# Performance work log

Hardware: AMD Instinct MI355X
Metric: run time of the kernel (lower is better)

## Reference

```python
import jax, jax.numpy as jnp
import numpy as np

N = 50000      # nodes
E = 600000     # edges
D = 128        # embedding_dim
H = 256        # GENConv MLP hidden = 2*D (expansion=2, num_layers=2)
L = 2          # n_layers
EPS_MSG = 1e-7
EPS_NORM = 1e-5


def setup_inputs() -> dict:
    key = jax.random.key(0)
    ks = jax.random.split(key, 16)
    s = 0.05
    inp = {}
    inp["x"] = jax.random.normal(ks[0], (N, 1), jnp.float32)
    inp["edge_index"] = jax.random.randint(ks[1], (2, E), 0, N)
    inp["edge_attr"] = jax.random.normal(ks[2], (E, 1), jnp.float32)
    # encoders
    inp["Wn"] = jax.random.normal(ks[3], (1, D), jnp.float32) * s
    inp["bn_b"] = jnp.zeros((D,), jnp.float32)
    inp["We"] = jax.random.normal(ks[4], (1, D), jnp.float32) * s
    inp["be"] = jnp.zeros((D,), jnp.float32)
    # per-layer BatchNorm affine
    inp["bn_gamma"] = jnp.ones((L, D), jnp.float32)
    inp["bn_beta"] = jnp.zeros((L, D), jnp.float32)
    # per-layer GENConv params: learnable temperature t, MLP [D->H->D] with LayerNorm
    inp["t"] = jnp.ones((L,), jnp.float32)
    inp["W1"] = jax.random.normal(ks[5], (L, D, H), jnp.float32) * s
    inp["b1"] = jnp.zeros((L, H), jnp.float32)
    inp["ln_g"] = jnp.ones((L, H), jnp.float32)
    inp["ln_b"] = jnp.zeros((L, H), jnp.float32)
    inp["W2"] = jax.random.normal(ks[6], (L, H, D), jnp.float32) * s
    inp["b2"] = jnp.zeros((L, D), jnp.float32)
    return inp


def _segment_softmax(logits, seg, num):
    # per-channel softmax over edges grouped by destination node
    m = jax.ops.segment_max(logits, seg, num_segments=num)
    m = jnp.where(jnp.isfinite(m), m, 0.0)  # empty segments
    ex = jnp.exp(logits - m[seg])
    den = jax.ops.segment_sum(ex, seg, num_segments=num)
    return ex / (den[seg] + 1e-16)


def reference(x, edge_index, edge_attr, Wn, bn_b, We, be,
              bn_gamma, bn_beta, t, W1, b1, ln_g, ln_b, W2, b2):
    src, dst = edge_index[0], edge_index[1]
    h = x @ Wn + bn_b                 # [N, D] node encoder
    e = edge_attr @ We + be           # [E, D] edge encoder
    for l in range(L):
        # DeepGCNLayer 'res+': h_in -> BN -> ReLU -> conv -> + h_in
        mu = h.mean(axis=0)
        var = h.var(axis=0)
        hn = (h - mu) / jnp.sqrt(var + EPS_NORM) * bn_gamma[l] + bn_beta[l]
        hn = jax.nn.relu(hn)
        # GENConv: msg = relu(x_j + e) + eps; softmax-aggr with temperature t
        msg = jax.nn.relu(hn[src] + e) + EPS_MSG          # [E, D]
        alpha = _segment_softmax(msg * t[l], dst, N)      # [E, D]
        agg = jax.ops.segment_sum(msg * alpha, dst, num_segments=N)  # [N, D]
        out = agg + hn                                    # add root
        # GENConv MLP: Linear -> LayerNorm -> ReLU -> Linear
        z = out @ W1[l] + b1[l]
        zm = z.mean(axis=-1, keepdims=True)
        zv = z.var(axis=-1, keepdims=True)
        z = (z - zm) / jnp.sqrt(zv + EPS_NORM) * ln_g[l] + ln_b[l]
        z = jax.nn.relu(z)
        z = z @ W2[l] + b2[l]
        h = h + z                                         # res+ residual
    # DotProductPredictor over the same edge list
    return (h[src] * h[dst]).sum(axis=-1)                 # [E]
```

## Files before the change

### kernel.cpp

```cpp
#include <hip/hip_runtime.h>
#include <hip/hip_bf16.h>
#include <math.h>

#define NN 50000
#define NE 600000
#define MPAD 50048
#define DIM 128
#define HID 256
#define EPS_MSG 1e-7f
#define EPS_NORM 1e-5f

typedef __attribute__((ext_vector_type(8))) short short8v;
typedef __attribute__((ext_vector_type(8))) unsigned short ushort8v;
typedef __attribute__((ext_vector_type(4))) float f32x4;

__device__ inline ushort f2bf(float f) {
    union { float f; unsigned u; } v; v.f = f;
    unsigned r = v.u + 0x7FFF + ((v.u >> 16) & 1);
    return (ushort)(r >> 16);
}
__device__ inline float bf2f(ushort u) {
    union { unsigned u; float f; } v; v.u = (unsigned)u << 16; return v.f;
}

__global__ void k_xstats(const float* __restrict__ x, float* __restrict__ xs, int n) {
    int lane = threadIdx.x & 63;
    float s = 0.f, q = 0.f;
    for (int i = blockIdx.x * blockDim.x + threadIdx.x; i < n; i += gridDim.x * blockDim.x) {
        float v = x[i];
        s += v; q += v * v;
    }
    #pragma unroll
    for (int off = 32; off >= 1; off >>= 1) {
        s += __shfl_xor(s, off, 64);
        q += __shfl_xor(q, off, 64);
    }
    if (lane == 0) { atomicAdd(&xs[0], s); atomicAdd(&xs[1], q); }
}

__global__ void k_hn0(const float* __restrict__ x, const float* __restrict__ xs,
                      const float* __restrict__ Wn, const float* __restrict__ bnb,
                      const float* __restrict__ gamma, const float* __restrict__ beta,
                      ushort* __restrict__ hn, int total4) {
    int i = blockIdx.x * blockDim.x + threadIdx.x;
    if (i >= total4) return;
    int d4 = (i & 31) * 4;
    int n = i >> 5;
    float mx = xs[0] * (1.f / NN);
    float vx = xs[1] * (1.f / NN) - mx * mx;
    float xv = x[n];
    float4 w = *(const float4*)(Wn + d4);
    float4 b = *(const float4*)(bnb + d4);
    float4 g = *(const float4*)(gamma + d4);
    float4 bt = *(const float4*)(beta + d4);
    ushort4 o;
    {
        float mu = fmaf(mx, w.x, b.x), sc = rsqrtf(vx * w.x * w.x + EPS_NORM) * g.x;
        o.x = f2bf(fmaxf(fmaf(fmaf(xv, w.x, b.x) - mu, sc, bt.x), 0.f));
    }
    {
        float mu = fmaf(mx, w.y, b.y), sc = rsqrtf(vx * w.y * w.y + EPS_NORM) * g.y;
        o.y = f2bf(fmaxf(fmaf(fmaf(xv, w.y, b.y) - mu, sc, bt.y), 0.f));
    }
    {
        float mu = fmaf(mx, w.z, b.z), sc = rsqrtf(vx * w.z * w.z + EPS_NORM) * g.z;
        o.z = f2bf(fmaxf(fmaf(fmaf(xv, w.z, b.z) - mu, sc, bt.z), 0.f));
    }
    {
        float mu = fmaf(mx, w.w, b.w), sc = rsqrtf(vx * w.w * w.w + EPS_NORM) * g.w;
        o.w = f2bf(fmaxf(fmaf(fmaf(xv, w.w, b.w) - mu, sc, bt.w), 0.f));
    }
    *(ushort4*)(hn + (size_t)n * DIM + d4) = o;
}

__global__ void k_castAll(const float* __restrict__ W1, const float* __restrict__ W2,
                          ushort* __restrict__ W1t, ushort* __restrict__ W2t) {
    const int chunk = DIM * HID;
    int i = blockIdx.x * blockDim.x + threadIdx.x;
    if (i >= 4 * chunk) return;
    int w = i / chunk;
    int j = i - w * chunk;
    if (w < 2) {
        int r = j / HID, c = j - r * HID;
        W1t[(size_t)w * chunk + (size_t)c * DIM + r] = f2bf(W1[(size_t)w * chunk + j]);
    } else {
        int l = w - 2;
        int r = j / DIM, c = j - r * DIM;
        W2t[(size_t)l * chunk + (size_t)c * HID + r] = f2bf(W2[(size_t)l * chunk + j]);
    }
}

__global__ void k_hist(const int* __restrict__ dst, int* __restrict__ deg, int E) {
    int i = blockIdx.x * blockDim.x + threadIdx.x;
    if (i < E) atomicAdd(&deg[dst[i]], 1);
}

__global__ __launch_bounds__(1024) void k_scan(const int* __restrict__ deg,
                                               int* __restrict__ row_off,
                                               int* __restrict__ cursor, int n) {
    __shared__ int wsum[16];
    __shared__ int carry;
    if (threadIdx.x == 0) carry = 0;
    __syncthreads();
    int lane = threadIdx.x & 63;
    int wid = threadIdx.x >> 6;
    for (int base = 0; base < n; base += 1024) {
        int i = base + (int)threadIdx.x;
        int v = (i < n) ? deg[i] : 0;
        int x = v;
        #pragma unroll
        for (int off = 1; off < 64; off <<= 1) {
            int y = __shfl_up(x, off, 64);
            if (lane >= off) x += y;
        }
        if (lane == 63) wsum[wid] = x;
        __syncthreads();
        if (wid == 0 && lane < 16) {
            int w = wsum[lane];
            #pragma unroll
            for (int off = 1; off < 16; off <<= 1) {
                int y = __shfl_up(w, off, 64);
                if (lane >= off) w += y;
            }
            wsum[lane] = w;
        }
        __syncthreads();
        int prev = (wid == 0) ? 0 : wsum[wid - 1];
        int excl = carry + prev + (x - v);
        if (i < n) { row_off[i] = excl; cursor[i] = excl; }
        int chunk_total = wsum[15];
        __syncthreads();
        if (threadIdx.x == 0) carry += chunk_total;
        __syncthreads();
    }
    if (threadIdx.x == 0) row_off[n] = carry;
}

__global__ void k_scatter(const int* __restrict__ src, const int* __restrict__ dst,
                          const float* __restrict__ eattr, int* __restrict__ cursor,
                          int* __restrict__ col_src, float* __restrict__ ea_perm,
                          int* __restrict__ eid, int E) {
    int i = blockIdx.x * blockDim.x + threadIdx.x;
    if (i >= E) return;
    int d = dst[i];
    int pos = atomicAdd(&cursor[d], 1);
    col_src[pos] = src[i];
    ea_perm[pos] = eattr[i];
    eid[pos] = i;
}

__global__ void k_bn_relu(const float* __restrict__ h, const float* __restrict__ stats,
                          const float* __restrict__ gamma, const float* __restrict__ beta,
                          ushort* __restrict__ hn, int total4) {
    int i = blockIdx.x * blockDim.x + threadIdx.x;
    if (i >= total4) return;
    int d4 = (i & 31) * 4;
    int n = i >> 5;
    float4 v = *(const float4*)(h + (size_t)n * DIM + d4);
    float4 s = *(const float4*)(stats + d4);
    float4 q = *(const float4*)(stats + DIM + d4);
    float4 g = *(const float4*)(gamma + d4);
    float4 bt = *(const float4*)(beta + d4);
    ushort4 o;
    {
        float mu = s.x * (1.f / NN), var = q.x * (1.f / NN) - mu * mu;
        float sc = rsqrtf(var + EPS_NORM) * g.x;
        o.x = f2bf(fmaxf(fmaf(v.x - mu, sc, bt.x), 0.f));
    }
    {
        float mu = s.y * (1.f / NN), var = q.y * (1.f / NN) - mu * mu;
        float sc = rsqrtf(var + EPS_NORM) * g.y;
        o.y = f2bf(fmaxf(fmaf(v.y - mu, sc, bt.y), 0.f));
    }
    {
        float mu = s.z * (1.f / NN), var = q.z * (1.f / NN) - mu * mu;
        float sc = rsqrtf(var + EPS_NORM) * g.z;
        o.z = f2bf(fmaxf(fmaf(v.z - mu, sc, bt.z), 0.f));
    }
    {
        float mu = s.w * (1.f / NN), var = q.w * (1.f / NN) - mu * mu;
        float sc = rsqrtf(var + EPS_NORM) * g.w;
        o.w = f2bf(fmaxf(fmaf(v.w - mu, sc, bt.w), 0.f));
    }
    *(ushort4*)(hn + (size_t)n * DIM + d4) = o;
}

__global__ __launch_bounds__(256) void k_agg(const ushort* __restrict__ hn,
                                             const float* __restrict__ ea_perm,
                                             const int* __restrict__ col_src,
                                             const int* __restrict__ row_off,
                                             const float* __restrict__ We,
                                             const float* __restrict__ be,
                                             const float* __restrict__ t_all, int l,
                                             ushort* __restrict__ ob, int N) {
    int n = blockIdx.x * 4 + (threadIdx.x >> 6);
    if (n >= N) return;
    int lane = threadIdx.x & 63;
    int d0 = lane * 2;
    float2 we = *(const float2*)(We + d0);
    float2 bd = *(const float2*)(be + d0);
    float t = t_all[l];
    int p0 = row_off[n], p1 = row_off[n + 1];
    int deg = p1 - p0;

    int mp = p0 + lane;
    int s_l = (mp < p1) ? col_src[mp] : 0;
    float ea_l = (mp < p1) ? ea_perm[mp] : 0.f;

    float den0 = 0.f, num0 = 0.f, den1 = 0.f, num1 = 0.f;
    int kmax = deg < 64 ? deg : 64;
    int k = 0;
    for (; k + 4 <= kmax; k += 4) {
        int sA = __shfl(s_l, k, 64), sB = __shfl(s_l, k + 1, 64);
        int sC = __shfl(s_l, k + 2, 64), sD = __shfl(s_l, k + 3, 64);
        float eA = __shfl(ea_l, k, 64), eB = __shfl(ea_l, k + 1, 64);
        float eC = __shfl(ea_l, k + 2, 64), eD = __shfl(ea_l, k + 3, 64);
        uint hA = *(const uint*)(hn + (size_t)sA * DIM + d0);
        uint hB = *(const uint*)(hn + (size_t)sB * DIM + d0);
        uint hC = *(const uint*)(hn + (size_t)sC * DIM + d0);
        uint hD = *(const uint*)(hn + (size_t)sD * DIM + d0);
        {
            float m0 = fmaxf(bf2f((ushort)hA) + fmaf(eA, we.x, bd.x), 0.f) + EPS_MSG;
            float m1 = fmaxf(bf2f((ushort)(hA >> 16)) + fmaf(eA, we.y, bd.y), 0.f) + EPS_MSG;
            float x0 = __expf(m0 * t), x1 = __expf(m1 * t);
            den0 += x0; num0 += m0 * x0; den1 += x1; num1 += m1 * x1;
        }
        {
            float m0 = fmaxf(bf2f((ushort)hB) + fmaf(eB, we.x, bd.x), 0.f) + EPS_MSG;
            float m1 = fmaxf(bf2f((ushort)(hB >> 16)) + fmaf(eB, we.y, bd.y), 0.f) + EPS_MSG;
            float x0 = __expf(m0 * t), x1 = __expf(m1 * t);
            den0 += x0; num0 += m0 * x0; den1 += x1; num1 += m1 * x1;
        }
        {
            float m0 = fmaxf(bf2f((ushort)hC) + fmaf(eC, we.x, bd.x), 0.f) + EPS_MSG;
            float m1 = fmaxf(bf2f((ushort)(hC >> 16)) + fmaf(eC, we.y, bd.y), 0.f) + EPS_MSG;
            float x0 = __expf(m0 * t), x1 = __expf(m1 * t);
            den0 += x0; num0 += m0 * x0; den1 += x1; num1 += m1 * x1;
        }
        {
            float m0 = fmaxf(bf2f((ushort)hD) + fmaf(eD, we.x, bd.x), 0.f) + EPS_MSG;
            float m1 = fmaxf(bf2f((ushort)(hD >> 16)) + fmaf(eD, we.y, bd.y), 0.f) + EPS_MSG;
            float x0 = __expf(m0 * t), x1 = __expf(m1 * t);
            den0 += x0; num0 += m0 * x0; den1 += x1; num1 += m1 * x1;
        }
    }
    for (; k < kmax; ++k) {
        int s = __shfl(s_l, k, 64);
        float ea = __shfl(ea_l, k, 64);
        uint hv = *(const uint*)(hn + (size_t)s * DIM + d0);
        float m0 = fmaxf(bf2f((ushort)hv) + fmaf(ea, we.x, bd.x), 0.f) + EPS_MSG;
        float m1 = fmaxf(bf2f((ushort)(hv >> 16)) + fmaf(ea, we.y, bd.y), 0.f) + EPS_MSG;
        float x0 = __expf(m0 * t), x1 = __expf(m1 * t);
        den0 += x0; num0 += m0 * x0; den1 += x1; num1 += m1 * x1;
    }
    for (int p = p0 + 64; p < p1; ++p) {
        int s = col_src[p];
        float ea = ea_perm[p];
        uint hv = *(const uint*)(hn + (size_t)s * DIM + d0);
        float m0 = fmaxf(bf2f((ushort)hv) + fmaf(ea, we.x, bd.x), 0.f) + EPS_MSG;
        float m1 = fmaxf(bf2f((ushort)(hv >> 16)) + fmaf(ea, we.y, bd.y), 0.f) + EPS_MSG;
        float x0 = __expf(m0 * t), x1 = __expf(m1 * t);
        den0 += x0; num0 += m0 * x0; den1 += x1; num1 += m1 * x1;
    }
    uint hr = *(const uint*)(hn + (size_t)n * DIM + d0);
    float a0 = (deg > 0) ? num0 / (den0 + 1e-16f) : 0.f;
    float a1 = (deg > 0) ? num1 / (den1 + 1e-16f) : 0.f;
    uint o = (uint)f2bf(a0 + bf2f((ushort)hr)) |
             ((uint)f2bf(a1 + bf2f((ushort)(hr >> 16))) << 16);
    *(uint*)(ob + (size_t)n * DIM + d0) = o;
}

__global__ __launch_bounds__(256) void k_gemm_ln(const ushort* __restrict__ A,
                                                 const ushort* __restrict__ Bt,
                                                 const float* __restrict__ b1,
                                                 const float* __restrict__ g,
                                                 const float* __restrict__ bv,
                                                 ushort* __restrict__ Z) {
    constexpr int LDT = 136;
    __shared__ ushort As[64 * LDT];
    __shared__ float red_s[4][64];
    __shared__ float red_q[4][64];
    __shared__ float murs[2][64];
    const int tid = threadIdx.x;
    const int lane = tid & 63;
    const int wid = tid >> 6;
    const int row0 = blockIdx.x * 64;
    const int wc = wid * 64;
    const int l15 = lane & 15;
    const int lq = lane >> 4;

    #pragma unroll
    for (int i = 0; i < 4; ++i) {
        int idx = tid + i * 256;
        int r = idx >> 4;
        int c8 = (idx & 15) * 8;
        *(float4*)(As + r * LDT + c8) = *(const float4*)(A + (size_t)(row0 + r) * DIM + c8);
    }
    __syncthreads();

    f32x4 acc[4][4] = {};
    #pragma unroll
    for (int ks = 0; ks < 4; ++ks) {
        int kk = ks * 32 + lq * 8;
        short8v bfr[4], afr[4];
        #pragma unroll
        for (int f = 0; f < 4; ++f)
            bfr[f] = *(const short8v*)(Bt + (size_t)(wc + f * 16 + l15) * DIM + kk);
        #pragma unroll
        for (int f = 0; f < 4; ++f)
            afr[f] = *(const short8v*)(As + (f * 16 + l15) * LDT + kk);
        #pragma unroll
        for (int mi = 0; mi < 4; ++mi)
            #pragma unroll
            for (int ni = 0; ni < 4; ++ni)
                acc[mi][ni] = __builtin_amdgcn_mfma_f32_16x16x32_bf16(
                    afr[mi], bfr[ni], acc[mi][ni], 0, 0, 0);
    }

    float bb[4], gg[4], bb2[4];
    #pragma unroll
    for (int ni = 0; ni < 4; ++ni) {
        int col = wc + ni * 16 + l15;
        bb[ni] = b1[col]; gg[ni] = g[col]; bb2[ni] = bv[col];
    }
    #pragma unroll
    for (int mi = 0; mi < 4; ++mi) {
        #pragma unroll
        for (int j = 0; j < 4; ++j) {
            float s = 0.f, q = 0.f;
            #pragma unroll
            for (int ni = 0; ni < 4; ++ni) {
                float v = acc[mi][ni][j] + bb[ni];
                acc[mi][ni][j] = v;
                s += v; q += v * v;
            }
            #pragma unroll
            for (int off = 1; off <= 8; off <<= 1) {
                s += __shfl_xor(s, off, 64);
                q += __shfl_xor(q, off, 64);
            }
            if (l15 == 0) {
                int row = mi * 16 + lq * 4 + j;
                red_s[wid][row] = s;
                red_q[wid][row] = q;
            }
        }
    }
    __syncthreads();
    if (tid < 64) {
        float s = red_s[0][tid] + red_s[1][tid] + red_s[2][tid] + red_s[3][tid];
        float q = red_q[0][tid] + red_q[1][tid] + red_q[2][tid] + red_q[3][tid];
        float mu = s * (1.f / HID);
        float var = q * (1.f / HID) - mu * mu;
        murs[0][tid] = mu;
        murs[1][tid] = rsqrtf(var + EPS_NORM);
    }
    __syncthreads();
    #pragma unroll
    for (int mi = 0; mi < 4; ++mi) {
        #pragma unroll
        for (int j = 0; j < 4; ++j) {
            int row = mi * 16 + lq * 4 + j;
            float mu = murs[0][row], rs = murs[1][row];
            #pragma unroll
            for (int ni = 0; ni < 4; ++ni) {
                float v = fmaxf(fmaf((acc[mi][ni][j] - mu) * rs, gg[ni], bb2[ni]), 0.f);
                Z[(size_t)(row0 + row) * HID + wc + ni * 16 + l15] = f2bf(v);
            }
        }
    }
}

template <int FIRST, int STATS, int OUTB>
__global__ __launch_bounds__(256, 2) void k_gemm2(const ushort* __restrict__ A,
                                                  const ushort* __restrict__ Bt,
                                                  const float* __restrict__ b2,
                                                  const float* __restrict__ x,
                                                  const float* __restrict__ Wn,
                                                  const float* __restrict__ bnb,
                                                  float* __restrict__ C,
                                                  ushort* __restrict__ hb,
                                                  float* __restrict__ stats) {
    constexpr int LDT = 136;
    constexpr int K = HID;
    __shared__ ushort As[128 * LDT];
    __shared__ ushort Bs[128 * LDT];
    const int tid = threadIdx.x;
    const int row0 = blockIdx.x * 128;
    const int wid = tid >> 6;
    const int lane = tid & 63;
    const int wr = (wid >> 1) * 64;
    const int wc = (wid & 1) * 64;
    const int l15 = lane & 15;
    const int lq = lane >> 4;
    f32x4 acc[4][4] = {};

    for (int k0 = 0; k0 < K; k0 += 128) {
        float4 va[8], vb[8];
        #pragma unroll
        for (int i = 0; i < 8; ++i) {
            int idx = tid + i * 256;
            int r = idx >> 4;
            int c8 = (idx & 15) * 8;
            va[i] = *(const float4*)(A + (size_t)(row0 + r) * K + k0 + c8);
            vb[i] = *(const float4*)(Bt + (size_t)r * K + k0 + c8);
        }
        if (k0) __syncthreads();
        #pragma unroll
        for (int i = 0; i < 8; ++i) {
            int idx = tid + i * 256;
            int r = idx >> 4;
            int c8 = (idx & 15) * 8;
            *(float4*)(As + r * LDT + c8) = va[i];
            *(float4*)(Bs + r * LDT + c8) = vb[i];
        }
        __syncthreads();
        #pragma unroll
        for (int ks = 0; ks < 4; ++ks) {
            int kk = ks * 32 + lq * 8;
            short8v af[4], bf[4];
            #pragma unroll
            for (int f = 0; f < 4; ++f) {
                af[f] = *(const short8v*)(As + (wr + f * 16 + l15) * LDT + kk);
                bf[f] = *(const short8v*)(Bs + (wc + f * 16 + l15) * LDT + kk);
            }
            #pragma unroll
            for (int mi = 0; mi < 4; ++mi)
                #pragma unroll
                for (int ni = 0; ni < 4; ++ni)
                    acc[mi][ni] = __builtin_amdgcn_mfma_f32_16x16x32_bf16(
                        af[mi], bf[ni], acc[mi][ni], 0, 0, 0);
        }
    }

    float ssum[4] = {0.f, 0.f, 0.f, 0.f};
    float sq[4] = {0.f, 0.f, 0.f, 0.f};
    #pragma unroll
    for (int ni = 0; ni < 4; ++ni) {
        int col = wc + ni * 16 + l15;
        float bvv = b2[col];
        float wnc = FIRST ? Wn[col] : 0.f;
        float bnc = FIRST ? bnb[col] : 0.f;
        #pragma unroll
        for (int mi = 0; mi < 4; ++mi) {
            int rowb = row0 + wr + mi * 16 + lq * 4;
            #pragma unroll
            for (int j = 0; j < 4; ++j) {
                int gr = rowb + j;
                float base;
                if (FIRST) {
                    float xv = (gr < NN) ? x[gr] : 0.f;
                    base = fmaf(xv, wnc, bnc);
                } else {
                    base = C[(size_t)gr * DIM + col];
                }
                float v = acc[mi][ni][j] + bvv + base;
                if (OUTB) hb[(size_t)gr * DIM + col] = f2bf(v);
                else C[(size_t)gr * DIM + col] = v;
                if (STATS) {
                    bool ok = gr < NN;
                    ssum[ni] += ok ? v : 0.f;
                    sq[ni] += ok ? v * v : 0.f;
                }
            }
        }
    }
    if (STATS) {
        #pragma unroll
        for (int ni = 0; ni < 4; ++ni) {
            float s = ssum[ni], q = sq[ni];
            s += __shfl_xor(s, 16, 64); s += __shfl_xor(s, 32, 64);
            q += __shfl_xor(q, 16, 64); q += __shfl_xor(q, 32, 64);
            if (lq == 0) {
                int col = wc + ni * 16 + l15;
                atomicAdd(&stats[col], s);
                atomicAdd(&stats[DIM + col], q);
            }
        }
    }
}

__global__ __launch_bounds__(256) void k_dot(const ushort* __restrict__ hb,
                                             const int* __restrict__ col_src,
                                             const int* __restrict__ eid,
                                             const int* __restrict__ row_off,
                                             float* __restrict__ out, int N) {
    int n = blockIdx.x * 4 + (threadIdx.x >> 6);
    if (n >= N) return;
    int lane = threadIdx.x & 63;
    int sub = lane >> 4;
    int l16 = lane & 15;
    float hd[8];
    {
        ushort8v hv = *(const ushort8v*)(hb + (size_t)n * DIM + l16 * 8);
        #pragma unroll
        for (int j = 0; j < 8; ++j) hd[j] = bf2f(hv[j]);
    }
    int p0 = row_off[n], p1 = row_off[n + 1];
    int deg = p1 - p0;
    int mp = p0 + lane;
    int s_l = (mp < p1) ? col_src[mp] : 0;
    int e_l = (mp < p1) ? eid[mp] : 0;
    int kmax = deg < 64 ? deg : 64;
    for (int k = 0; k < kmax; k += 4) {
        int idx = k + sub;
        bool ok = idx < kmax;
        int s = __shfl(s_l, idx, 64);
        int e = __shfl(e_l, idx, 64);
        ushort8v av = *(const ushort8v*)(hb + (size_t)(ok ? s : n) * DIM + l16 * 8);
        float p = 0.f;
        #pragma unroll
        for (int j = 0; j < 8; ++j) p = fmaf(bf2f(av[j]), hd[j], p);
        p += __shfl_xor(p, 1, 16);
        p += __shfl_xor(p, 2, 16);
        p += __shfl_xor(p, 4, 16);
        p += __shfl_xor(p, 8, 16);
        if (ok && l16 == 0) out[e] = p;
    }
    for (int pb = p0 + 64; pb < p1; pb += 4) {
        int pe = pb + sub;
        bool ok = pe < p1;
        int s = ok ? col_src[pe] : n;
        int e = ok ? eid[pe] : 0;
        ushort8v av = *(const ushort8v*)(hb + (size_t)s * DIM + l16 * 8);
        float p = 0.f;
        #pragma unroll
        for (int j = 0; j < 8; ++j) p = fmaf(bf2f(av[j]), hd[j], p);
        p += __shfl_xor(p, 1, 16);
        p += __shfl_xor(p, 2, 16);
        p += __shfl_xor(p, 4, 16);
        p += __shfl_xor(p, 8, 16);
        if (ok && l16 == 0) out[e] = p;
    }
}

extern "C" void kernel_launch(void* const* d_in, const int* in_sizes, int n_in,
                              void* d_out, int out_size, void* d_ws, size_t ws_size,
                              hipStream_t stream) {
    const float* x        = (const float*)d_in[0];
    const int*   ei       = (const int*)d_in[1];
    const float* eattr    = (const float*)d_in[2];
    const float* Wn       = (const float*)d_in[3];
    const float* bnb      = (const float*)d_in[4];
    const float* We       = (const float*)d_in[5];
    const float* be       = (const float*)d_in[6];
    const float* bn_gamma = (const float*)d_in[7];
    const float* bn_beta  = (const float*)d_in[8];
    const float* t_all    = (const float*)d_in[9];
    const float* W1       = (const float*)d_in[10];
    const float* b1       = (const float*)d_in[11];
    const float* ln_g     = (const float*)d_in[12];
    const float* ln_b     = (const float*)d_in[13];
    const float* W2       = (const float*)d_in[14];
    const float* b2       = (const float*)d_in[15];
    float* out = (float*)d_out;

    const int N = NN, E = NE, D = DIM, H = HID;
    const int* src = ei;
    const int* dst = ei + E;

    char* ws = (char*)d_ws;
    auto alloc = [&](size_t bytes) {
        char* p = ws;
        ws += (bytes + 255) & ~(size_t)255;
        return p;
    };
    float*  h       = (float*)alloc((size_t)MPAD * D * 4);
    ushort* z1r     = (ushort*)alloc((size_t)MPAD * H * 2);
    ushort* ob      = (ushort*)alloc((size_t)MPAD * D * 2);
    ushort* hn      = (ushort*)alloc((size_t)MPAD * D * 2);
    ushort* hb      = (ushort*)alloc((size_t)MPAD * D * 2);
    ushort* W1t     = (ushort*)alloc((size_t)2 * D * H * 2);
    ushort* W2t     = (ushort*)alloc((size_t)2 * D * H * 2);
    int*    col_src = (int*)alloc((size_t)E * 4);
    float*  ea_perm = (float*)alloc((size_t)E * 4);
    int*    eid     = (int*)alloc((size_t)E * 4);
    int*    row_off = (int*)alloc((size_t)(N + 1) * 4);
    int*    cursor  = (int*)alloc((size_t)N * 4);
    int*    deg     = (int*)alloc((size_t)N * 4);
    float*  stats   = (float*)alloc((size_t)2 * D * 4);
    float*  xs      = (float*)alloc((size_t)2 * 4);

    hipMemsetAsync(deg, 0, (size_t)N * 4, stream);
    hipMemsetAsync(stats, 0, 1024 + 8, stream);

    k_xstats<<<64, 256, 0, stream>>>(x, xs, N);
    k_castAll<<<(4 * D * H + 255) / 256, 256, 0, stream>>>(W1, W2, W1t, W2t);
    k_hist<<<(E + 255) / 256, 256, 0, stream>>>(dst, deg, E);
    k_scan<<<1, 1024, 0, stream>>>(deg, row_off, cursor, N);
    k_scatter<<<(E + 255) / 256, 256, 0, stream>>>(src, dst, eattr, cursor,
                                                   col_src, ea_perm, eid, E);
    k_hn0<<<(N * 32 + 255) / 256, 256, 0, stream>>>(x, xs, Wn, bnb, bn_gamma, bn_beta,
                                                    hn, N * 32);

    k_agg<<<(N + 3) / 4, 256, 0, stream>>>(hn, ea_perm, col_src, row_off, We, be,
                                           t_all, 0, ob, N);
    k_gemm_ln<<<MPAD / 64, 256, 0, stream>>>(ob, W1t, b1, ln_g, ln_b, z1r);
    k_gemm2<1, 1, 0><<<MPAD / 128, 256, 0, stream>>>(z1r, W2t, b2, x, Wn, bnb, h, hb, stats);
    k_bn_relu<<<(N * 32 + 255) / 256, 256, 0, stream>>>(h, stats, bn_gamma + D, bn_beta + D,
                                                        hn, N * 32);

    k_agg<<<(N + 3) / 4, 256, 0, stream>>>(hn, ea_perm, col_src, row_off, We, be,
                                           t_all, 1, ob, N);
    k_gemm_ln<<<MPAD / 64, 256, 0, stream>>>(ob, W1t + (size_t)D * H, b1 + H,
                                             ln_g + H, ln_b + H, z1r);
    k_gemm2<0, 0, 1><<<MPAD / 128, 256, 0, stream>>>(z1r, W2t + (size_t)D * H, b2 + D,
                                                     x, Wn, bnb, h, hb, stats);

    k_dot<<<(N + 3) / 4, 256, 0, stream>>>(hb, col_src, eid, row_off, out, N);
}
```

Baseline: 445.4 us.

## Fuse MLP GEMMs through shared memory, pack edge records, parallelize scan

Merges the two MLP GEMM kernels into one per-layer kernel that keeps the LayerNorm/ReLU hidden activations in shared memory, so the bf16 intermediate never makes a round trip through global memory. Edge source, id and attribute are packed into one int4 record per CSR slot, replacing three separate arrays. The single-block prefix scan becomes a three-kernel multi-block scan. The costs are larger per-edge record reads (16 bytes instead of 8 or 12), A-fragments read directly from global memory, and more shared memory per block.

Result: faster. 390.8 us (-12.3%).

```diff
diff --git a/kernel.cpp b/kernel.cpp
--- a/kernel.cpp
+++ b/kernel.cpp
@@ -7,6 +7,7 @@
 #define MPAD 50048
 #define DIM 128
 #define HID 256
+#define NB 49
 #define EPS_MSG 1e-7f
 #define EPS_NORM 1e-5f
 
@@ -95,58 +96,79 @@
     if (i < E) atomicAdd(&deg[dst[i]], 1);
 }
 
-__global__ __launch_bounds__(1024) void k_scan(const int* __restrict__ deg,
-                                               int* __restrict__ row_off,
-                                               int* __restrict__ cursor, int n) {
+__global__ __launch_bounds__(256) void k_scanA(const int* __restrict__ deg,
+                                               int* __restrict__ partials, int n) {
+    __shared__ int ws[4];
+    int b = blockIdx.x;
+    int t = threadIdx.x;
+    int s = 0;
+    #pragma unroll
+    for (int i = 0; i < 4; ++i) {
+        int idx = b * 1024 + t + i * 256;
+        s += (idx < n) ? deg[idx] : 0;
+    }
+    #pragma unroll
+    for (int off = 32; off >= 1; off >>= 1) s += __shfl_xor(s, off, 64);
+    if ((t & 63) == 0) ws[t >> 6] = s;
+    __syncthreads();
+    if (t == 0) partials[b] = ws[0] + ws[1] + ws[2] + ws[3];
+}
+
+__global__ __launch_bounds__(64) void k_scanB(const int* __restrict__ partials,
+                                              int* __restrict__ base,
+                                              int* __restrict__ row_off) {
+    int t = threadIdx.x;
+    int v = (t < NB) ? partials[t] : 0;
+    int x = v;
+    #pragma unroll
+    for (int off = 1; off < 64; off <<= 1) {
+        int y = __shfl_up(x, off, 64);
+        if (t >= off) x += y;
+    }
+    if (t < NB) base[t] = x - v;
+    if (t == 0) row_off[NN] = NE;
+}
+
+__global__ __launch_bounds__(1024) void k_scanC(const int* __restrict__ deg,
+                                                const int* __restrict__ base,
+                                                int* __restrict__ row_off,
+                                                int* __restrict__ cursor, int n) {
     __shared__ int wsum[16];
-    __shared__ int carry;
-    if (threadIdx.x == 0) carry = 0;
-    __syncthreads();
+    int i = blockIdx.x * 1024 + threadIdx.x;
     int lane = threadIdx.x & 63;
     int wid = threadIdx.x >> 6;
-    for (int base = 0; base < n; base += 1024) {
-        int i = base + (int)threadIdx.x;
-        int v = (i < n) ? deg[i] : 0;
-        int x = v;
-        #pragma unroll
-        for (int off = 1; off < 64; off <<= 1) {
-            int y = __shfl_up(x, off, 64);
-            if (lane >= off) x += y;
-        }
-        if (lane == 63) wsum[wid] = x;
-        __syncthreads();
-        if (wid == 0 && lane < 16) {
-            int w = wsum[lane];
-            #pragma unroll
-            for (int off = 1; off < 16; off <<= 1) {
-                int y = __shfl_up(w, off, 64);
-                if (lane >= off) w += y;
-            }
-            wsum[lane] = w;
-        }
-        __syncthreads();
-        int prev = (wid == 0) ? 0 : wsum[wid - 1];
-        int excl = carry + prev + (x - v);
-        if (i < n) { row_off[i] = excl; cursor[i] = excl; }
-        int chunk_total = wsum[15];
-        __syncthreads();
-        if (threadIdx.x == 0) carry += chunk_total;
-        __syncthreads();
-    }
-    if (threadIdx.x == 0) row_off[n] = carry;
+    int v = (i < n) ? deg[i] : 0;
+    int x = v;
+    #pragma unroll
+    for (int off = 1; off < 64; off <<= 1) {
+        int y = __shfl_up(x, off, 64);
+        if (lane >= off) x += y;
+    }
+    if (lane == 63) wsum[wid] = x;
+    __syncthreads();
+    if (wid == 0 && lane < 16) {
+        int w = wsum[lane];
+        #pragma unroll
+        for (int off = 1; off < 16; off <<= 1) {
+            int y = __shfl_up(w, off, 64);
+            if (lane >= off) w += y;
+        }
+        wsum[lane] = w;
+    }
+    __syncthreads();
+    int prev = (wid == 0) ? 0 : wsum[wid - 1];
+    int excl = base[blockIdx.x] + prev + (x - v);
+    if (i < n) { row_off[i] = excl; cursor[i] = excl; }
 }
 
 __global__ void k_scatter(const int* __restrict__ src, const int* __restrict__ dst,
                           const float* __restrict__ eattr, int* __restrict__ cursor,
-                          int* __restrict__ col_src, float* __restrict__ ea_perm,
-                          int* __restrict__ eid, int E) {
+                          int4* __restrict__ erec, int E) {
     int i = blockIdx.x * blockDim.x + threadIdx.x;
     if (i >= E) return;
     int d = dst[i];
     int pos = atomicAdd(&cursor[d], 1);
-    col_src[pos] = src[i];
-    ea_perm[pos] = eattr[i];
-    eid[pos] = i;
+    erec[pos] = make_int4(src[i], i, __float_as_int(eattr[i]), 0);
 }
 
 __global__ void k_bn_relu(const float* __restrict__ h, const float* __restrict__ stats,
@@ -186,8 +208,7 @@
 }
 
 __global__ __launch_bounds__(256) void k_agg(const ushort* __restrict__ hn,
-                                             const float* __restrict__ ea_perm,
-                                             const int* __restrict__ col_src,
+                                             const int4* __restrict__ erec,
                                              const int* __restrict__ row_off,
                                              const float* __restrict__ We,
                                              const float* __restrict__ be,
@@ -204,8 +225,11 @@
     int deg = p1 - p0;
 
     int mp = p0 + lane;
-    int s_l = (mp < p1) ? col_src[mp] : 0;
-    float ea_l = (mp < p1) ? ea_perm[mp] : 0.f;
+    int s_l = 0; float ea_l = 0.f;
+    if (mp < p1) {
+        int4 r = erec[mp];
+        s_l = r.x; ea_l = __int_as_float(r.z);
+    }
 
     float den0 = 0.f, num0 = 0.f, den1 = 0.f, num1 = 0.f;
     int kmax = deg < 64 ? deg : 64;
@@ -254,8 +278,9 @@
         den0 += x0; num0 += m0 * x0; den1 += x1; num1 += m1 * x1;
     }
     for (int p = p0 + 64; p < p1; ++p) {
-        int s = col_src[p];
-        float ea = ea_perm[p];
+        int4 r = erec[p];
+        int s = r.x;
+        float ea = __int_as_float(r.z);
         uint hv = *(const uint*)(hn + (size_t)s * DIM + d0);
         float m0 = fmaxf(bf2f((ushort)hv) + fmaf(ea, we.x, bd.x), 0.f) + EPS_MSG;
         float m1 = fmaxf(bf2f((ushort)(hv >> 16)) + fmaf(ea, we.y, bd.y), 0.f) + EPS_MSG;
@@ -270,14 +295,22 @@
     *(uint*)(ob + (size_t)n * DIM + d0) = o;
 }
 
-__global__ __launch_bounds__(256) void k_gemm_ln(const ushort* __restrict__ A,
-                                                 const ushort* __restrict__ Bt,
-                                                 const float* __restrict__ b1,
-                                                 const float* __restrict__ g,
-                                                 const float* __restrict__ bv,
-                                                 ushort* __restrict__ Z) {
-    constexpr int LDT = 136;
-    __shared__ ushort As[64 * LDT];
+template <int FIRST>
+__global__ __launch_bounds__(256) void k_mlp(const ushort* __restrict__ A,
+                                             const ushort* __restrict__ B1t,
+                                             const float* __restrict__ b1,
+                                             const float* __restrict__ g,
+                                             const float* __restrict__ bv,
+                                             const ushort* __restrict__ B2t,
+                                             const float* __restrict__ b2,
+                                             const float* __restrict__ x,
+                                             const float* __restrict__ Wn,
+                                             const float* __restrict__ bnb,
+                                             float* __restrict__ C,
+                                             ushort* __restrict__ hb,
+                                             float* __restrict__ stats) {
+    constexpr int LDZ = 264;
+    __shared__ ushort Zs[64 * LDZ];
     __shared__ float red_s[4][64];
     __shared__ float red_q[4][64];
     __shared__ float murs[2][64];
@@ -289,15 +322,6 @@
     const int l15 = lane & 15;
     const int lq = lane >> 4;
 
-    #pragma unroll
-    for (int i = 0; i < 4; ++i) {
-        int idx = tid + i * 256;
-        int r = idx >> 4;
-        int c8 = (idx & 15) * 8;
-        *(float4*)(As + r * LDT + c8) = *(const float4*)(A + (size_t)(row0 + r) * DIM + c8);
-    }
-    __syncthreads();
-
     f32x4 acc[4][4] = {};
     #pragma unroll
     for (int ks = 0; ks < 4; ++ks) {
@@ -305,10 +329,10 @@
         short8v bfr[4], afr[4];
         #pragma unroll
         for (int f = 0; f < 4; ++f)
-            bfr[f] = *(const short8v*)(Bt + (size_t)(wc + f * 16 + l15) * DIM + kk);
+            bfr[f] = *(const short8v*)(B1t + (size_t)(wc + f * 16 + l15) * DIM + kk);
         #pragma unroll
         for (int f = 0; f < 4; ++f)
-            afr[f] = *(const short8v*)(As + (f * 16 + l15) * LDT + kk);
+            afr[f] = *(const short8v*)(A + (size_t)(row0 + f * 16 + l15) * DIM + kk);
         #pragma unroll
         for (int mi = 0; mi < 4; ++mi)
             #pragma unroll
@@ -365,85 +389,43 @@
             #pragma unroll
             for (int ni = 0; ni < 4; ++ni) {
                 float v = fmaxf(fmaf((acc[mi][ni][j] - mu) * rs, gg[ni], bb2[ni]), 0.f);
-                Z[(size_t)(row0 + row) * HID + wc + ni * 16 + l15] = f2bf(v);
+                Zs[row * LDZ + wc + ni * 16 + l15] = f2bf(v);
             }
         }
     }
-}
-
-template <int FIRST, int STATS, int OUTB>
-__global__ __launch_bounds__(256, 2) void k_gemm2(const ushort* __restrict__ A,
-                                                  const ushort* __restrict__ Bt,
-                                                  const float* __restrict__ b2,
-                                                  const float* __restrict__ x,
-                                                  const float* __restrict__ Wn,
-                                                  const float* __restrict__ bnb,
-                                                  float* __restrict__ C,
-                                                  ushort* __restrict__ hb,
-                                                  float* __restrict__ stats) {
-    constexpr int LDT = 136;
-    constexpr int K = HID;
-    __shared__ ushort As[128 * LDT];
-    __shared__ ushort Bs[128 * LDT];
-    const int tid = threadIdx.x;
-    const int row0 = blockIdx.x * 128;
-    const int wid = tid >> 6;
-    const int lane = tid & 63;
-    const int wr = (wid >> 1) * 64;
-    const int wc = (wid & 1) * 64;
-    const int l15 = lane & 15;
-    const int lq = lane >> 4;
-    f32x4 acc[4][4] = {};
-
-    for (int k0 = 0; k0 < K; k0 += 128) {
-        float4 va[8], vb[8];
-        #pragma unroll
-        for (int i = 0; i < 8; ++i) {
-            int idx = tid + i * 256;
-            int r = idx >> 4;
-            int c8 = (idx & 15) * 8;
-            va[i] = *(const float4*)(A + (size_t)(row0 + r) * K + k0 + c8);
-            vb[i] = *(const float4*)(Bt + (size_t)r * K + k0 + c8);
-        }
-        if (k0) __syncthreads();
-        #pragma unroll
-        for (int i = 0; i < 8; ++i) {
-            int idx = tid + i * 256;
-            int r = idx >> 4;
-            int c8 = (idx & 15) * 8;
-            *(float4*)(As + r * LDT + c8) = va[i];
-            *(float4*)(Bs + r * LDT + c8) = vb[i];
-        }
-        __syncthreads();
-        #pragma unroll
-        for (int ks = 0; ks < 4; ++ks) {
-            int kk = ks * 32 + lq * 8;
-            short8v af[4], bf[4];
+    __syncthreads();
+
+    const int wc2 = wid * 32;
+    f32x4 acc2[4][2] = {};
+    #pragma unroll
+    for (int ks = 0; ks < 8; ++ks) {
+        int kk = ks * 32 + lq * 8;
+        short8v bf2[2], af2[4];
+        #pragma unroll
+        for (int f = 0; f < 2; ++f)
+            bf2[f] = *(const short8v*)(B2t + (size_t)(wc2 + f * 16 + l15) * HID + kk);
+        #pragma unroll
+        for (int f = 0; f < 4; ++f)
+            af2[f] = *(const short8v*)(Zs + (f * 16 + l15) * LDZ + kk);
+        #pragma unroll
+        for (int mi = 0; mi < 4; ++mi)
             #pragma unroll
-            for (int f = 0; f < 4; ++f) {
-                af[f] = *(const short8v*)(As + (wr + f * 16 + l15) * LDT + kk);
-                bf[f] = *(const short8v*)(Bs + (wc + f * 16 + l15) * LDT + kk);
-            }
-            #pragma unroll
-            for (int mi = 0; mi < 4; ++mi)
-                #pragma unroll
-                for (int ni = 0; ni < 4; ++ni)
-                    acc[mi][ni] = __builtin_amdgcn_mfma_f32_16x16x32_bf16(
-                        af[mi], bf[ni], acc[mi][ni], 0, 0, 0);
-        }
-    }
-
-    float ssum[4] = {0.f, 0.f, 0.f, 0.f};
-    float sq[4] = {0.f, 0.f, 0.f, 0.f};
-    #pragma unroll
-    for (int ni = 0; ni < 4; ++ni) {
-        int col = wc + ni * 16 + l15;
+            for (int ni = 0; ni < 2; ++ni)
+                acc2[mi][ni] = __builtin_amdgcn_mfma_f32_16x16x32_bf16(
+                    af2[mi], bf2[ni], acc2[mi][ni], 0, 0, 0);
+    }
+
+    float ssum[2] = {0.f, 0.f};
+    float sq[2] = {0.f, 0.f};
+    #pragma unroll
+    for (int ni = 0; ni < 2; ++ni) {
+        int col = wc2 + ni * 16 + l15;
         float bvv = b2[col];
         float wnc = FIRST ? Wn[col] : 0.f;
         float bnc = FIRST ? bnb[col] : 0.f;
         #pragma unroll
         for (int mi = 0; mi < 4; ++mi) {
-            int rowb = row0 + wr + mi * 16 + lq * 4;
+            int rowb = row0 + mi * 16 + lq * 4;
             #pragma unroll
             for (int j = 0; j < 4; ++j) {
                 int gr = rowb + j;
@@ -454,25 +436,26 @@
                 } else {
                     base = C[(size_t)gr * DIM + col];
                 }
-                float v = acc[mi][ni][j] + bvv + base;
-                if (OUTB) hb[(size_t)gr * DIM + col] = f2bf(v);
-                else C[(size_t)gr * DIM + col] = v;
-                if (STATS) {
+                float v = acc2[mi][ni][j] + bvv + base;
+                if (FIRST) {
+                    C[(size_t)gr * DIM + col] = v;
                     bool ok = gr < NN;
                     ssum[ni] += ok ? v : 0.f;
                     sq[ni] += ok ? v * v : 0.f;
+                } else {
+                    hb[(size_t)gr * DIM + col] = f2bf(v);
                 }
             }
         }
     }
-    if (STATS) {
-        #pragma unroll
-        for (int ni = 0; ni < 4; ++ni) {
+    if (FIRST) {
+        #pragma unroll
+        for (int ni = 0; ni < 2; ++ni) {
             float s = ssum[ni], q = sq[ni];
             s += __shfl_xor(s, 16, 64); s += __shfl_xor(s, 32, 64);
             q += __shfl_xor(q, 16, 64); q += __shfl_xor(q, 32, 64);
             if (lq == 0) {
-                int col = wc + ni * 16 + l15;
+                int col = wc2 + ni * 16 + l15;
                 atomicAdd(&stats[col], s);
                 atomicAdd(&stats[DIM + col], q);
             }
@@ -481,8 +464,7 @@
 }
 
 __global__ __launch_bounds__(256) void k_dot(const ushort* __restrict__ hb,
-                                             const int* __restrict__ col_src,
-                                             const int* __restrict__ eid,
+                                             const int4* __restrict__ erec,
                                              const int* __restrict__ row_off,
                                              float* __restrict__ out, int N) {
     int n = blockIdx.x * 4 + (threadIdx.x >> 6);
@@ -499,8 +481,11 @@
     int p0 = row_off[n], p1 = row_off[n + 1];
     int deg = p1 - p0;
     int mp = p0 + lane;
-    int s_l = (mp < p1) ? col_src[mp] : 0;
-    int e_l = (mp < p1) ? eid[mp] : 0;
+    int s_l = 0, e_l = 0;
+    if (mp < p1) {
+        int4 r = erec[mp];
+        s_l = r.x; e_l = r.y;
+    }
     int kmax = deg < 64 ? deg : 64;
     for (int k = 0; k < kmax; k += 4) {
         int idx = k + sub;
@@ -520,8 +505,8 @@
     for (int pb = p0 + 64; pb < p1; pb += 4) {
         int pe = pb + sub;
         bool ok = pe < p1;
-        int s = ok ? col_src[pe] : n;
-        int e = ok ? eid[pe] : 0;
+        int s = n, e = 0;
+        if (ok) { int4 r = erec[pe]; s = r.x; e = r.y; }
         ushort8v av = *(const ushort8v*)(hb + (size_t)s * DIM + l16 * 8);
         float p = 0.f;
         #pragma unroll
@@ -566,18 +551,17 @@
         return p;
     };
     float*  h       = (float*)alloc((size_t)MPAD * D * 4);
-    ushort* z1r     = (ushort*)alloc((size_t)MPAD * H * 2);
     ushort* ob      = (ushort*)alloc((size_t)MPAD * D * 2);
     ushort* hn      = (ushort*)alloc((size_t)MPAD * D * 2);
     ushort* hb      = (ushort*)alloc((size_t)MPAD * D * 2);
     ushort* W1t     = (ushort*)alloc((size_t)2 * D * H * 2);
     ushort* W2t     = (ushort*)alloc((size_t)2 * D * H * 2);
-    int*    col_src = (int*)alloc((size_t)E * 4);
-    float*  ea_perm = (float*)alloc((size_t)E * 4);
-    int*    eid     = (int*)alloc((size_t)E * 4);
+    int4*   erec    = (int4*)alloc((size_t)E * 16);
     int*    row_off = (int*)alloc((size_t)(N + 1) * 4);
     int*    cursor  = (int*)alloc((size_t)N * 4);
     int*    deg     = (int*)alloc((size_t)N * 4);
+    int*    partials= (int*)alloc((size_t)64 * 4);
+    int*    pbase   = (int*)alloc((size_t)64 * 4);
     float*  stats   = (float*)alloc((size_t)2 * D * 4);
     float*  xs      = (float*)alloc((size_t)2 * 4);
 
@@ -587,25 +571,23 @@
     k_xstats<<<64, 256, 0, stream>>>(x, xs, N);
     k_castAll<<<(4 * D * H + 255) / 256, 256, 0, stream>>>(W1, W2, W1t, W2t);
     k_hist<<<(E + 255) / 256, 256, 0, stream>>>(dst, deg, E);
-    k_scan<<<1, 1024, 0, stream>>>(deg, row_off, cursor, N);
-    k_scatter<<<(E + 255) / 256, 256, 0, stream>>>(src, dst, eattr, cursor,
-                                                   col_src, ea_perm, eid, E);
+    k_scanA<<<NB, 256, 0, stream>>>(deg, partials, N);
+    k_scanB<<<1, 64, 0, stream>>>(partials, pbase, row_off);
+    k_scanC<<<NB, 1024, 0, stream>>>(deg, pbase, row_off, cursor, N);
+    k_scatter<<<(E + 255) / 256, 256, 0, stream>>>(src, dst, eattr, cursor, erec, E);
     k_hn0<<<(N * 32 + 255) / 256, 256, 0, stream>>>(x, xs, Wn, bnb, bn_gamma, bn_beta,
                                                     hn, N * 32);
 
-    k_agg<<<(N + 3) / 4, 256, 0, stream>>>(hn, ea_perm, col_src, row_off, We, be,
-                                           t_all, 0, ob, N);
-    k_gemm_ln<<<MPAD / 64, 256, 0, stream>>>(ob, W1t, b1, ln_g, ln_b, z1r);
-    k_gemm2<1, 1, 0><<<MPAD / 128, 256, 0, stream>>>(z1r, W2t, b2, x, Wn, bnb, h, hb, stats);
+    k_agg<<<(N + 3) / 4, 256, 0, stream>>>(hn, erec, row_off, We, be, t_all, 0, ob, N);
+    k_mlp<1><<<MPAD / 64, 256, 0, stream>>>(ob, W1t, b1, ln_g, ln_b, W2t, b2,
+                                            x, Wn, bnb, h, hb, stats);
     k_bn_relu<<<(N * 32 + 255) / 256, 256, 0, stream>>>(h, stats, bn_gamma + D, bn_beta + D,
                                                         hn, N * 32);
 
-    k_agg<<<(N + 3) / 4, 256, 0, stream>>>(hn, ea_perm, col_src, row_off, We, be,
-                                           t_all, 1, ob, N);
-    k_gemm_ln<<<MPAD / 64, 256, 0, stream>>>(ob, W1t + (size_t)D * H, b1 + H,
-                                             ln_g + H, ln_b + H, z1r);
-    k_gemm2<0, 0, 1><<<MPAD / 128, 256, 0, stream>>>(z1r, W2t + (size_t)D * H, b2 + D,
-                                                     x, Wn, bnb, h, hb, stats);
-
-    k_dot<<<(N + 3) / 4, 256, 0, stream>>>(hb, col_src, eid, row_off, out, N);
-}
+    k_agg<<<(N + 3) / 4, 256, 0, stream>>>(hn, erec, row_off, We, be, t_all, 1, ob, N);
+    k_mlp<0><<<MPAD / 64, 256, 0, stream>>>(ob, W1t + (size_t)D * H, b1 + H,
+                                            ln_g + H, ln_b + H, W2t + (size_t)D * H, b2 + D,
+                                            x, Wn, bnb, h, hb, stats);
+
+    k_dot<<<(N + 3) / 4, 256, 0, stream>>>(hb, erec, row_off, out, N);
+}
```
